# Kernel optimization log

Hardware: AMD Instinct MI355X
Metric: run time of the kernel (lower is better)

Reference implementation:

```python
import math
import jax, jax.numpy as jnp
import numpy as np

B, T, E, H = 4, 2048, 1024, 16
S = E // H
SCALE = 1.0 / math.sqrt(S)
LN_EPS = 1e-5


def setup_inputs() -> dict:
    key = jax.random.key(0)
    ks = jax.random.split(key, 5)
    w_std = 1.0 / math.sqrt(E)
    return {
        "x": jax.random.normal(ks[0], (B, T, E), jnp.float32),
        "Wq": jax.random.normal(ks[1], (E, E), jnp.float32) * w_std,
        "Wk": jax.random.normal(ks[2], (E, E), jnp.float32) * w_std,
        "Wv": jax.random.normal(ks[3], (E, E), jnp.float32) * w_std,
        "Wu": jax.random.normal(ks[4], (E, E), jnp.float32) * w_std,
        "bu": jnp.zeros((E,), jnp.float32),
        "q_gamma": jnp.ones((S,), jnp.float32),
        "q_beta": jnp.zeros((S,), jnp.float32),
        "k_gamma": jnp.ones((S,), jnp.float32),
        "k_beta": jnp.zeros((S,), jnp.float32),
    }


def _layernorm(x, gamma, beta):
    # normalize over last (head) dim, eps matches torch LayerNorm default
    mu = jnp.mean(x, axis=-1, keepdims=True)
    var = jnp.mean(jnp.square(x - mu), axis=-1, keepdims=True)
    return (x - mu) * jax.lax.rsqrt(var + LN_EPS) * gamma + beta


def reference(x, Wq, Wk, Wv, Wu, bu, q_gamma, q_beta, k_gamma, k_beta):
    b, t, e = x.shape
    h, s = H, S
    # torch Linear: y = x @ W^T ; split into heads [b, t, h, s]
    q = (x @ Wq.T).reshape(b, t, h, s)
    k = (x @ Wk.T).reshape(b, t, h, s)
    v = (x @ Wv.T).reshape(b, t, h, s)
    # kqnorm: LayerNorm over head dim s
    q = _layernorm(q, q_gamma, q_beta)
    k = _layernorm(k, k_gamma, k_beta)
    # scaled dot-product scores [b, h, t, t]
    dots = jnp.einsum("bthd,bThd->bhtT", q, k) * SCALE
    causal = jnp.tril(jnp.ones((t, t), dtype=bool))
    dots = jnp.where(causal, dots, jnp.finfo(dots.dtype).min)
    attn = jax.nn.softmax(dots, axis=-1)
    out = jnp.einsum("bhtT,bThd->bthd", attn, v).reshape(b, t, e)
    return out @ Wu.T + bu
```

## Files before the change

### kernel.cpp

```cpp
#include <hip/hip_runtime.h>
#include <hip/hip_bf16.h>
#include <stdint.h>
#include <stddef.h>


using bf16 = __hip_bfloat16;
typedef __attribute__((ext_vector_type(8))) short s16x8;
typedef __attribute__((ext_vector_type(4))) short s16x4;
typedef __attribute__((ext_vector_type(4))) float f32x4;

#define MFMA16(a, b, c) __builtin_amdgcn_mfma_f32_16x16x32_bf16((a), (b), (c), 0, 0, 0)

static __device__ __forceinline__ s16x8 ld8(const bf16* p) {
    return *reinterpret_cast<const s16x8*>(p);
}
static __device__ __forceinline__ s16x8 ld8s(const short* p) {
    return *reinterpret_cast<const s16x8*>(p);
}
static __device__ __forceinline__ s16x8 cvt8(const float* p) {
    f32x4 u = *reinterpret_cast<const f32x4*>(p);
    f32x4 v = *reinterpret_cast<const f32x4*>(p + 4);
    s16x8 r;
#pragma unroll
    for (int e = 0; e < 4; e++) {
        r[e]     = __builtin_bit_cast(short, __float2bfloat16(u[e]));
        r[e + 4] = __builtin_bit_cast(short, __float2bfloat16(v[e]));
    }
    return r;
}
static __device__ __forceinline__ unsigned int cvtpk(float lo, float hi) {
    unsigned int r;
    asm("v_cvt_pk_bf16_f32 %0, %1, %2" : "=v"(r) : "v"(lo), "v"(hi));
    return r;
}

static __device__ __forceinline__ void async16(short* lds, const bf16* g) {
    __builtin_amdgcn_global_load_lds(
        (const __attribute__((address_space(1))) unsigned int*)g,
        (__attribute__((address_space(3))) unsigned int*)lds, 16, 0, 0);
}

#define EE 1024

__global__ __launch_bounds__(256) void cvt_all(
    const float* __restrict__ w0, const float* __restrict__ w1,
    const float* __restrict__ w2, const float* __restrict__ w3,
    const float* __restrict__ x,
    bf16* __restrict__ o0, bf16* __restrict__ o1,
    bf16* __restrict__ o2, bf16* __restrict__ o3, bf16* __restrict__ xb)
{
    const int z = blockIdx.z;
    const float* s;
    bf16* d;
    if (z < 4) {
        s = (z == 0) ? w0 : (z == 1) ? w1 : (z == 2) ? w2 : w3;
        d = (z == 0) ? o0 : (z == 1) ? o1 : (z == 2) ? o2 : o3;
    } else {
        s = x  + (size_t)(z - 4) * 1048576;
        d = xb + (size_t)(z - 4) * 1048576;
    }
    size_t i = ((size_t)blockIdx.x * 256 + threadIdx.x) * 8;
    *reinterpret_cast<s16x8*>(d + i) = cvt8(s + i);
}

template <int AF32>
__global__ __launch_bounds__(256, AF32 ? 1 : 3) void gemm_qkv_t(
    const float* __restrict__ xf, const bf16* __restrict__ xb,
    const bf16* __restrict__ Wq, const bf16* __restrict__ Wk, const bf16* __restrict__ Wv,
    bf16* __restrict__ Qb, bf16* __restrict__ Kb, bf16* __restrict__ Vb,
    const float* __restrict__ qg, const float* __restrict__ qbt,
    const float* __restrict__ kg, const float* __restrict__ kbt)
{
    const int z = blockIdx.z;
    const bf16* Bt = (z == 0) ? Wq : (z == 1) ? Wk : Wv;
    bf16* out      = (z == 0) ? Qb : (z == 1) ? Kb : Vb;
    const float* gamma = (z == 0) ? qg : kg;
    const float* beta  = (z == 0) ? qbt : kbt;
    const bool  ln     = (z < 2);
    const float oscale = (z == 0) ? 0.125f * 1.44269504088896340736f : 1.0f;

    constexpr int LASZ = AF32 ? 128 * 40 : 2 * 4096;
    __shared__ __align__(16) short lA[LASZ];
    __shared__ __align__(16) short lB[2 * 4096];

    const int tid  = threadIdx.x;
    const int lane = tid & 63;
    const int w    = tid >> 6;
    const int wr = w >> 1, wc = w & 1;
    const int lr = lane & 15, quad = lane >> 4;

    const int mi = blockIdx.x * 8 + (blockIdx.y & 7);
    const int ni = blockIdx.y >> 3;
    const int m0 = mi * 128;
    const int n0 = ni * 128;

    const int strow = w * 32 + (lane >> 2);
    const int stcol = AF32 ? (lane & 3) * 8
                           : (((lane & 3) ^ (strow & 3)) << 3);
    const bf16* bgl = Bt + (size_t)(n0 + strow) * EE + stcol;

    f32x4 acc[4][4];
#pragma unroll
    for (int i = 0; i < 4; i++)
#pragma unroll
        for (int j = 0; j < 4; j++) acc[i][j] = (f32x4){0.f, 0.f, 0.f, 0.f};

    if constexpr (AF32) {
        constexpr int SA = 40;
        const int sr  = tid >> 1;
        const int sc0 = (tid & 1) << 4;
        const float* ap = xf + (size_t)(m0 + sr) * EE + sc0;
        short* lap = lA + sr * SA + sc0;
        short* bl = lB + (w * 2) * 512;
        const short* lArd = lA + (wr * 64 + lr) * SA + quad * 8;
        const short* lBrd = lB + (wc * 64 + lr) * 32 + quad * 8;
        const bf16* bg = bgl;

        for (int kt = 0; kt < EE / 32; ++kt) {
            s16x8 a0 = cvt8(ap), a1 = cvt8(ap + 8);
            __syncthreads();
            *reinterpret_cast<s16x8*>(lap)     = a0;
            *reinterpret_cast<s16x8*>(lap + 8) = a1;
            async16(bl, bg);
            async16(bl + 512, bg + 16 * EE);
            ap += 32;
            bg += 32;
            __syncthreads();

            s16x8 af[4], bfr[4];
#pragma unroll
            for (int i = 0; i < 4; i++) af[i]  = ld8s(lArd + i * 16 * SA);
#pragma unroll
            for (int j = 0; j < 4; j++) bfr[j] = ld8s(lBrd + j * 16 * 32);
#pragma unroll
            for (int i = 0; i < 4; i++)
#pragma unroll
                for (int j = 0; j < 4; j++) acc[i][j] = MFMA16(af[i], bfr[j], acc[i][j]);
        }
    } else {
        const bf16* agl = xb + (size_t)(m0 + strow) * EE + stcol;
        short* const al0 = lA + w * 1024;
        short* const bl0 = lB + w * 1024;

#define QSTAGE(c, kt)                                                     \
    {                                                                     \
        short* al = al0 + (c) * 4096;                                     \
        short* bl = bl0 + (c) * 4096;                                     \
        const bf16* ag = agl + (kt) * 32;                                 \
        const bf16* bg = bgl + (kt) * 32;                                 \
        async16(al, ag); async16(al + 512, ag + 16 * EE);                 \
        async16(bl, bg); async16(bl + 512, bg + 16 * EE);                 \
    }

        QSTAGE(0, 0)
        const int ard = (wr * 64 + lr) * 32 + ((quad ^ (lr & 3)) << 3);
        const int brd = (wc * 64 + lr) * 32 + ((quad ^ (lr & 3)) << 3);
#pragma unroll 1
        for (int kt = 0; kt < EE / 32; ++kt) {
            const int c = kt & 1;
            if (kt < EE / 32 - 1) {
                QSTAGE(c ^ 1, kt + 1)
                asm volatile("s_waitcnt vmcnt(4)" ::: "memory");
            } else {
                asm volatile("s_waitcnt vmcnt(0)" ::: "memory");
            }
            __builtin_amdgcn_s_barrier();

            const short* lArd = lA + c * 4096 + ard;
            const short* lBrd = lB + c * 4096 + brd;
            s16x8 af[4], bfr[4];
#pragma unroll
            for (int i = 0; i < 4; i++) af[i]  = ld8s(lArd + i * 512);
#pragma unroll
            for (int j = 0; j < 4; j++) bfr[j] = ld8s(lBrd + j * 512);
#pragma unroll
            for (int i = 0; i < 4; i++)
#pragma unroll
                for (int j = 0; j < 4; j++) acc[i][j] = MFMA16(af[i], bfr[j], acc[i][j]);
            __builtin_amdgcn_s_barrier();
        }
#undef QSTAGE
    }

    if (ln) {
        float g[4], bt[4];
#pragma unroll
        for (int j = 0; j < 4; j++) {
            g[j]  = gamma[j * 16 + lr];
            bt[j] = beta[j * 16 + lr];
        }
#pragma unroll
        for (int i = 0; i < 4; i++) {
#pragma unroll
            for (int r = 0; r < 4; r++) {
                float s1 = 0.f, s2 = 0.f;
#pragma unroll
                for (int j = 0; j < 4; j++) {
                    float v = acc[i][j][r];
                    s1 += v;
                    s2 += v * v;
                }
#pragma unroll
                for (int off = 1; off < 16; off <<= 1) {
                    s1 += __shfl_xor(s1, off);
                    s2 += __shfl_xor(s2, off);
                }
                float mu  = s1 * (1.f / 64.f);
                float var = s2 * (1.f / 64.f) - mu * mu;
                float rs  = rsqrtf(var + 1e-5f);
                int row = m0 + wr * 64 + i * 16 + quad * 4 + r;
#pragma unroll
                for (int j = 0; j < 4; j++) {
                    float v = ((acc[i][j][r] - mu) * rs * g[j] + bt[j]) * oscale;
                    out[(size_t)row * EE + n0 + wc * 64 + j * 16 + lr] = __float2bfloat16(v);
                }
            }
        }
    } else {
#pragma unroll
        for (int i = 0; i < 4; i++)
#pragma unroll
            for (int r = 0; r < 4; r++) {
                int row = m0 + wr * 64 + i * 16 + quad * 4 + r;
#pragma unroll
                for (int j = 0; j < 4; j++)
                    out[(size_t)row * EE + n0 + wc * 64 + j * 16 + lr] =
                        __float2bfloat16(acc[i][j][r]);
            }
    }
}

__global__ __launch_bounds__(512, 4) void flash(
    const bf16* __restrict__ Qb, const bf16* __restrict__ Kb,
    const bf16* __restrict__ Vb, bf16* __restrict__ Ob)
{
    const int flat = blockIdx.y * 8 + blockIdx.x;
    const int vid  = (flat & 7) * 64 + (flat >> 3);
    const int pr = vid & 7;
    const int bh = vid >> 3;
    const int b = bh >> 4, h = bh & 15;
    const int tid = threadIdx.x, lane = tid & 63, w = tid >> 6;
    const int lr = lane & 15, quad = lane >> 4;
    const size_t base = (size_t)b * 2048 * 1024 + h * 64;

    __shared__ __align__(16) short VT[64 * 64];
    __shared__ __align__(16) short PT[128 * 64];
    __shared__ __align__(16) short KS[2][64 * 64];

    short* const prow = PT + (w * 16 + lr) * 64;
    const int lr7 = lr & 7;
    const bf16* const kst = Kb + base + (size_t)(w * 8 + (lane >> 3)) * 1024 +
                            (((lane & 7) ^ (lane >> 3)) << 3);
    short* const kdst = &KS[0][0] + w * 512;
    const int kaddr0 = lr * 64 + ((quad ^ lr7) << 3);

#pragma unroll 1
    for (int ph = 0; ph < 2; ++ph) {
        const int qt = ph ? (15 - pr) : pr;
        const int tw = qt * 128 + w * 16;

        s16x8 qf[2];
#pragma unroll
        for (int ks = 0; ks < 2; ks++)
            qf[ks] = ld8(Qb + base + (size_t)(tw + lr) * 1024 + ks * 32 + quad * 8);

        f32x4 o[4];
#pragma unroll
        for (int j = 0; j < 4; j++) o[j] = (f32x4){0.f, 0.f, 0.f, 0.f};
        float lsum = 0.f;

        const int nkt = 2 * qt + 2;

        __syncthreads();
        s16x8 va0 = ld8(Vb + base + (size_t)lane * 1024 + w * 8);
        s16x8 vb0;
        async16(kdst, kst);

#define FTILE(KT, V0C, KCUR, V0N, KNXT)                                          \
    {                                                                            \
        const int kb = (KT) * 64;                                                \
        const bool active = (kb <= tw + 15);                                     \
        asm volatile("s_waitcnt vmcnt(0)" ::: "memory");      \
        __builtin_amdgcn_s_barrier();       \
        _Pragma("unroll")                                                        \
        for (int e = 0; e < 8; e++)          \
            VT[(w * 8 + e) * 64 + (((lane >> 3) ^ e) << 3) + (lane & 7)]         \
                = V0C[e];                                                        \
        const int kb2 = kb + 64;                                                 \
        if (kb2 < nkt * 64) {       \
            async16(kdst + (KNXT) * 4096, kst + (size_t)kb2 * 1024);             \
            V0N = ld8(Vb + base + (size_t)(kb2 + lane) * 1024 + w * 8);          \
        }                                                                        \
        if (active) {                                                            \
            const short* kc = &KS[KCUR][0];                                      \
            f32x4 sc[4];                                                         \
            _Pragma("unroll")                                                    \
            for (int jk = 0; jk < 4; jk++) sc[jk] = (f32x4){0.f, 0.f, 0.f, 0.f}; \
            __builtin_amdgcn_s_setprio(1);                                       \
            _Pragma("unroll")                                                    \
            for (int ks = 0; ks < 2; ks++)                                       \
                _Pragma("unroll")                                                \
                for (int jk = 0; jk < 4; jk++) {                                 \
                    s16x8 kf = ld8s(kc + jk * 1024 + (kaddr0 ^ (ks * 32)));      \
                    sc[jk] = MFMA16(kf, qf[ks], sc[jk]);                         \
                }                                                                \
            __builtin_amdgcn_s_setprio(0);                                       \
            if (kb + 63 > tw) {                  \
                const int qq = tw + lr;                                          \
                _Pragma("unroll")                                                \
                for (int jk = 0; jk < 4; jk++) {                                 \
                    const int k0 = kb + jk * 16 + quad * 4;                      \
                    float p0 = exp2f(sc[jk][0]);                                 \
                    float p1 = exp2f(sc[jk][1]);                                 \
                    float p2 = exp2f(sc[jk][2]);                                 \
                    float p3 = exp2f(sc[jk][3]);                                 \
                    if (k0 + 0 > qq) p0 = 0.f;                                   \
                    if (k0 + 1 > qq) p1 = 0.f;                                   \
                    if (k0 + 2 > qq) p2 = 0.f;                                   \
                    if (k0 + 3 > qq) p3 = 0.f;                                   \
                    lsum += (p0 + p1) + (p2 + p3);                               \
                    uint2 pk = {cvtpk(p0, p1), cvtpk(p2, p3)};                   \
                    *reinterpret_cast<uint2*>(                                   \
                        prow + (((jk * 2 + (quad >> 1)) ^ lr7) << 3) +           \
                        ((quad & 1) << 2)) = pk;                                 \
                }                                                                \
            } else {                                 \
                _Pragma("unroll")                                                \
                for (int jk = 0; jk < 4; jk++) {                                 \
                    float p0 = exp2f(sc[jk][0]);                                 \
                    float p1 = exp2f(sc[jk][1]);                                 \
                    float p2 = exp2f(sc[jk][2]);                                 \
                    float p3 = exp2f(sc[jk][3]);                                 \
                    lsum += (p0 + p1) + (p2 + p3);                               \
                    uint2 pk = {cvtpk(p0, p1), cvtpk(p2, p3)};                   \
                    *reinterpret_cast<uint2*>(                                   \
                        prow + (((jk * 2 + (quad >> 1)) ^ lr7) << 3) +           \
                        ((quad & 1) << 2)) = pk;                                 \
                }                                                                \
            }                                                                    \
        }                                                                        \
        asm volatile("s_waitcnt lgkmcnt(0)" ::: "memory");    \
        __builtin_amdgcn_s_barrier();                  \
        if (active) {                                                            \
            _Pragma("unroll")                                                    \
            for (int ks = 0; ks < 2; ks++) {                                     \
                s16x8 pf = ld8s(prow + (((ks * 4 + quad) ^ lr7) << 3));          \
                s16x8 vf[4];                                                     \
                _Pragma("unroll")                                                \
                for (int j = 0; j < 4; j++)                                      \
                    vf[j] = ld8s(VT + (j * 16 + lr) * 64 +                       \
                                 (((ks * 4 + quad) ^ lr7) << 3));                \
                __builtin_amdgcn_s_setprio(1);                                   \
                _Pragma("unroll")                                                \
                for (int j = 0; j < 4; j++)                                      \
                    o[j] = MFMA16(pf, vf[j], o[j]);                              \
                __builtin_amdgcn_s_setprio(0);                                   \
            }                                                                    \
        }                                                                        \
    }

#pragma unroll 1
        for (int kt = 0; kt < nkt; kt += 2) {
            FTILE(kt,     va0, 0, vb0, 1)
            FTILE(kt + 1, vb0, 1, va0, 0)
        }
#undef FTILE

        float l = lsum;
        l += __shfl_xor(l, 16);
        l += __shfl_xor(l, 32);
#pragma unroll
        for (int r = 0; r < 4; r++) {
            float inv = 1.f / __shfl(l, quad * 4 + r);
            int t = tw + quad * 4 + r;
#pragma unroll
            for (int j = 0; j < 4; j++)
                Ob[base + (size_t)t * 1024 + j * 16 + lr] =
                    __float2bfloat16(o[j][r] * inv);
        }
    }
}

__global__ __launch_bounds__(256, 4) void gemm_bias(
    const bf16* __restrict__ A, const bf16* __restrict__ Bt,
    const float* __restrict__ bias, float* __restrict__ out)
{
    __shared__ __align__(16) short lA[2 * 2048];
    __shared__ __align__(16) short lB[2 * 4096];

    const int tid  = threadIdx.x;
    const int lane = tid & 63;
    const int w    = tid >> 6;
    const int lr = lane & 15, quad = lane >> 4;

    const int mi = blockIdx.x * 16 + (blockIdx.y & 15);
    const int ni = blockIdx.y >> 4;
    const int m0 = mi * 64;
    const int n0 = ni * 128;

    const int srA = w * 16 + (lane >> 2);
    const int srB = w * 32 + (lane >> 2);
    const bf16* agl = A  + (size_t)(m0 + srA) * EE + (((lane & 3) ^ (srA & 3)) << 3);
    const bf16* bgl = Bt + (size_t)(n0 + srB) * EE + (((lane & 3) ^ (srB & 3)) << 3);
    short* const al0 = lA + w * 512;
    short* const bl0 = lB + w * 1024;

    f32x4 acc[4][2];
#pragma unroll
    for (int i = 0; i < 4; i++)
#pragma unroll
        for (int j = 0; j < 2; j++) acc[i][j] = (f32x4){0.f, 0.f, 0.f, 0.f};

#define BSTAGE(c, kt)                                                     \
    {                                                                     \
        const bf16* ag = agl + (kt) * 32;                                 \
        const bf16* bg = bgl + (kt) * 32;                                 \
        async16(al0 + (c) * 2048, ag);                                    \
        async16(bl0 + (c) * 4096, bg);                                    \
        async16(bl0 + (c) * 4096 + 512, bg + 16 * EE);                    \
    }

    BSTAGE(0, 0)
    const int ard = lr * 32 + ((quad ^ (lr & 3)) << 3);
    const int brd = (w * 32 + lr) * 32 + ((quad ^ (lr & 3)) << 3);
#pragma unroll 1
    for (int kt = 0; kt < EE / 32; ++kt) {
        const int c = kt & 1;
        if (kt < EE / 32 - 1) {
            BSTAGE(c ^ 1, kt + 1)
            asm volatile("s_waitcnt vmcnt(3)" ::: "memory");
        } else {
            asm volatile("s_waitcnt vmcnt(0)" ::: "memory");
        }
        __builtin_amdgcn_s_barrier();

        const short* lArd = lA + c * 2048 + ard;
        const short* lBrd = lB + c * 4096 + brd;
        s16x8 af[4], bfr[2];
#pragma unroll
        for (int i = 0; i < 4; i++) af[i]  = ld8s(lArd + i * 512);
#pragma unroll
        for (int j = 0; j < 2; j++) bfr[j] = ld8s(lBrd + j * 512);
#pragma unroll
        for (int i = 0; i < 4; i++)
#pragma unroll
            for (int j = 0; j < 2; j++) acc[i][j] = MFMA16(af[i], bfr[j], acc[i][j]);
        __builtin_amdgcn_s_barrier();
    }
#undef BSTAGE

    float bz[2];
#pragma unroll
    for (int j = 0; j < 2; j++)
        bz[j] = bias[n0 + w * 32 + j * 16 + lr];
#pragma unroll
    for (int i = 0; i < 4; i++)
#pragma unroll
        for (int r = 0; r < 4; r++) {
            int row = m0 + i * 16 + quad * 4 + r;
#pragma unroll
            for (int j = 0; j < 2; j++)
                out[(size_t)row * EE + n0 + w * 32 + j * 16 + lr] =
                    acc[i][j][r] + bz[j];
        }
}

extern "C" void kernel_launch(void* const* d_in, const int* in_sizes, int n_in,
                              void* d_out, int out_size, void* d_ws, size_t ws_size,
                              hipStream_t stream)
{
    (void)in_sizes; (void)n_in; (void)out_size;
    const float* x   = (const float*)d_in[0];
    const float* Wq  = (const float*)d_in[1];
    const float* Wk  = (const float*)d_in[2];
    const float* Wv  = (const float*)d_in[3];
    const float* Wu  = (const float*)d_in[4];
    const float* bu  = (const float*)d_in[5];
    const float* qg  = (const float*)d_in[6];
    const float* qbt = (const float*)d_in[7];
    const float* kg  = (const float*)d_in[8];
    const float* kbt = (const float*)d_in[9];
    float* out = (float*)d_out;

    bf16* Qb  = (bf16*)d_ws;
    bf16* Kb  = Qb  + (size_t)8192 * 1024;
    bf16* Vb  = Kb  + (size_t)8192 * 1024;
    bf16* Wqb = Vb  + (size_t)8192 * 1024;
    bf16* Wkb = Wqb + (size_t)1024 * 1024;
    bf16* Wvb = Wkb + (size_t)1024 * 1024;
    bf16* Wub = Wvb + (size_t)1024 * 1024;
    bf16* xb  = Wub + (size_t)1024 * 1024;

    const size_t need = ((size_t)3 * 8192 * 1024 + 4 * 1024 * 1024 + 8192 * 1024) * 2;
    const bool fast = ws_size >= need;

    cvt_all<<<dim3(512, 1, fast ? 12 : 4), 256, 0, stream>>>(
        Wq, Wk, Wv, Wu, x, Wqb, Wkb, Wvb, Wub, xb);
    if (fast)
        gemm_qkv_t<0><<<dim3(8, 64, 3), 256, 0, stream>>>(
            x, xb, Wqb, Wkb, Wvb, Qb, Kb, Vb, qg, qbt, kg, kbt);
    else
        gemm_qkv_t<1><<<dim3(8, 64, 3), 256, 0, stream>>>(
            x, nullptr, Wqb, Wkb, Wvb, Qb, Kb, Vb, qg, qbt, kg, kbt);
    flash<<<dim3(8, 64), 512, 0, stream>>>(Qb, Kb, Vb, Qb);
    gemm_bias<<<dim3(8, 128), 256, 0, stream>>>(Qb, Wub, bu, out);
}
```

Before: 260.2 us.

## Double-buffer V tile in LDS to drop the per-tile second barrier

Makes the transposed V tile in shared memory double-buffered and writes the next tile's V one step ahead, with V global loads issued two tiles in advance. The P·V stage now reads the current buffer right after a local lgkmcnt wait, which removes the second workgroup barrier in each key tile. The cost is 8 KB more LDS per block. That can cut the number of resident blocks per CU under `launch_bounds(512,4)`, and it adds register pressure from holding prefetched V.

```diff
diff --git a/kernel.cpp b/kernel.cpp
--- a/kernel.cpp
+++ b/kernel.cpp
@@ -243,7 +243,7 @@
     const int lr = lane & 15, quad = lane >> 4;
     const size_t base = (size_t)b * 2048 * 1024 + h * 64;
 
-    __shared__ __align__(16) short VT[64 * 64];
+    __shared__ __align__(16) short VT[2][64 * 64];
     __shared__ __align__(16) short PT[128 * 64];
     __shared__ __align__(16) short KS[2][64 * 64];
 
@@ -272,25 +272,29 @@
         const int nkt = 2 * qt + 2;
 
         __syncthreads();
-        s16x8 va0 = ld8(Vb + base + (size_t)lane * 1024 + w * 8);
-        s16x8 vb0;
         async16(kdst, kst);
-
-#define FTILE(KT, V0C, KCUR, V0N, KNXT)                                          \
+        s16x8 va = ld8(Vb + base + (size_t)lane * 1024 + w * 8);
+        s16x8 vb = ld8(Vb + base + (size_t)(64 + lane) * 1024 + w * 8);
+        asm volatile("s_waitcnt vmcnt(1)" ::: "memory");
+#pragma unroll
+        for (int e = 0; e < 8; e++)
+            VT[0][(w * 8 + e) * 64 + (((lane >> 3) ^ e) << 3) + (lane & 7)] = va[e];
+
+#define FTILE(KT, VWR, KCUR, VLD)                                                \
     {                                                                            \
         const int kb = (KT) * 64;                                                \
         const bool active = (kb <= tw + 15);                                     \
-        asm volatile("s_waitcnt vmcnt(0)" ::: "memory");      \
-        __builtin_amdgcn_s_barrier();       \
+        asm volatile("s_waitcnt vmcnt(0) lgkmcnt(0)" ::: "memory");              \
+        __builtin_amdgcn_s_barrier();    \
         _Pragma("unroll")                                                        \
-        for (int e = 0; e < 8; e++)          \
-            VT[(w * 8 + e) * 64 + (((lane >> 3) ^ e) << 3) + (lane & 7)]         \
-                = V0C[e];                                                        \
-        const int kb2 = kb + 64;                                                 \
-        if (kb2 < nkt * 64) {       \
-            async16(kdst + (KNXT) * 4096, kst + (size_t)kb2 * 1024);             \
-            V0N = ld8(Vb + base + (size_t)(kb2 + lane) * 1024 + w * 8);          \
-        }                                                                        \
+        for (int e = 0; e < 8; e++)           \
+            VT[(KCUR) ^ 1][(w * 8 + e) * 64 + (((lane >> 3) ^ e) << 3) +         \
+                           (lane & 7)] = VWR[e];                                 \
+        const int kb2 = kb + 64, kb3 = kb + 128;                                 \
+        if (kb2 < nkt * 64)                  \
+            async16(kdst + ((KCUR) ^ 1) * 4096, kst + (size_t)kb2 * 1024);       \
+        if (kb3 < nkt * 64)                                  \
+            VLD = ld8(Vb + base + (size_t)(kb3 + lane) * 1024 + w * 8);          \
         if (active) {                                                            \
             const short* kc = &KS[KCUR][0];                                      \
             f32x4 sc[4];                                                         \
@@ -338,17 +342,15 @@
                         ((quad & 1) << 2)) = pk;                                 \
                 }                                                                \
             }                                                                    \
-        }                                                                        \
-        asm volatile("s_waitcnt lgkmcnt(0)" ::: "memory");    \
-        __builtin_amdgcn_s_barrier();                  \
-        if (active) {                                                            \
+            asm volatile("s_waitcnt lgkmcnt(0)" ::: "memory");  \
+            __builtin_amdgcn_sched_barrier(0);                                   \
             _Pragma("unroll")                                                    \
             for (int ks = 0; ks < 2; ks++) {                                     \
                 s16x8 pf = ld8s(prow + (((ks * 4 + quad) ^ lr7) << 3));          \
                 s16x8 vf[4];                                                     \
                 _Pragma("unroll")                                                \
                 for (int j = 0; j < 4; j++)                                      \
-                    vf[j] = ld8s(VT + (j * 16 + lr) * 64 +                       \
+                    vf[j] = ld8s(&VT[KCUR][0] + (j * 16 + lr) * 64 +             \
                                  (((ks * 4 + quad) ^ lr7) << 3));                \
                 __builtin_amdgcn_s_setprio(1);                                   \
                 _Pragma("unroll")                                                \
@@ -361,8 +363,8 @@
 
 #pragma unroll 1
         for (int kt = 0; kt < nkt; kt += 2) {
-            FTILE(kt,     va0, 0, vb0, 1)
-            FTILE(kt + 1, vb0, 1, va0, 0)
+            FTILE(kt,     vb, 0, va)
+            FTILE(kt + 1, va, 1, vb)
         }
 #undef FTILE
 
```

After: 261.3 us. Within noise of the previous version (+0.4%).
